# Kernel tuning notes

Measured on AMD Instinct MI355X. Metric: run time of the kernel, lower is better.

## Reference

```python
import jax, jax.numpy as jnp
import numpy as np

NPOINT, NSAMPLE, NKNN = 512, 16, 16


def _fps(xyz, npoint):
    # furthest point sampling. xyz: (B, N, 3) -> idx (B, npoint). Start at index 0 (as in pointnet2 CUDA op).
    B, N, _ = xyz.shape
    def body(carry, _):
        min_d, farthest = carry
        centroid = jnp.take_along_axis(xyz, farthest[:, None, None], axis=1)  # (B,1,3)
        d = jnp.sum((xyz - centroid) ** 2, axis=-1)                            # (B,N)
        min_d = jnp.minimum(min_d, d)
        nxt = jnp.argmax(min_d, axis=-1).astype(jnp.int32)
        return (min_d, nxt), farthest
    init = (jnp.full((B, N), 1e10, xyz.dtype), jnp.zeros((B,), jnp.int32))
    _, idx = jax.lax.scan(body, init, None, length=npoint)
    return jnp.transpose(idx)  # (B, npoint)


def _knn_idx(k, ref, query):
    # k nearest neighbors of each query point among ref points. ref:(B,N,3) query:(B,M,3) -> (B,M,k)
    d = (jnp.sum(query ** 2, -1, keepdims=True)
         - 2.0 * jnp.einsum('bmc,bnc->bmn', query, ref)
         + jnp.sum(ref ** 2, -1)[:, None, :])
    _, idx = jax.lax.top_k(-d, k)
    return idx


def _group(points, idx):
    # grouping_operation: points (B,C,N), idx (B,M,K) -> (B,C,M,K)
    return jax.vmap(lambda p, i: p[:, i])(points, idx)


def _conv1d(x, w, b):  # 1x1 conv: x (B,Cin,N), w (Cout,Cin)
    return jnp.einsum('oc,bcn->bon', w, x) + b[None, :, None]


def _conv2d(x, w, b):  # 1x1 conv: x (B,Cin,M,K)
    return jnp.einsum('oc,bcmk->bomk', w, x) + b[None, :, None, None]


def _linear(x, w, b):
    return x @ w.T + b


def _lrelu(x):
    return jnp.where(x >= 0, x, 0.2 * x)


def _model(point_cloud, sa_w1, sa_b1, sa_w2, sa_b2,
           t_start_w, t_start_b, t_q_w, t_q_b, t_k_w, t_k_b, t_v_w, t_v_b,
           t_pos_w1, t_pos_b1, t_pos_w2, t_pos_b2,
           t_attn_w1, t_attn_b1, t_attn_w2, t_attn_b2, t_end_w, t_end_b,
           exp_w1, exp_b1, exp_w2, exp_b2,
           mlp_w1, mlp_b1, mlp_w2, mlp_b2, mlp_w3, mlp_b3, mlp_w4, mlp_b4):
    B = point_cloud.shape[0]
    xyz = jnp.transpose(point_cloud, (0, 2, 1))                 # (B,N,3)

    # ---- PointNet_SA_Module_KNN (sample_and_group_knn, use_xyz=True) ----
    fps_idx = _fps(xyz, NPOINT)
    new_xyz = jnp.take_along_axis(xyz, fps_idx[:, :, None], axis=1)   # (B,512,3)
    idx = _knn_idx(NSAMPLE, xyz, new_xyz)                             # (B,512,16)
    grouped = _group(point_cloud, idx)                                # (B,3,512,16)
    grouped_xyz_rel = grouped - jnp.transpose(new_xyz, (0, 2, 1))[:, :, :, None]
    new_points = jnp.concatenate([grouped_xyz_rel, grouped], axis=1)  # (B,6,512,16)
    h = jax.nn.relu(_conv2d(new_points, sa_w1, sa_b1))
    h = _conv2d(h, sa_w2, sa_b2)                                      # (B,128,512,16)
    keyfeatures = jnp.max(h, axis=3)                                  # (B,128,512)
    keypoints = jnp.transpose(new_xyz, (0, 2, 1))                     # (B,3,512)

    # ---- point Transformer (BatchNorm in eval with default stats == identity) ----
    identity = keyfeatures
    x = _conv1d(keyfeatures, t_start_w, t_start_b)                    # (B,64,512)
    pos = keypoints
    pos_f = jnp.transpose(pos, (0, 2, 1))                             # (B,512,3)
    idx_knn = _knn_idx(NKNN, pos_f, pos_f)                            # (B,512,16)
    key_g = _group(_conv1d(x, t_k_w, t_k_b), idx_knn)                 # (B,64,512,16)
    value = _conv1d(x, t_v_w, t_v_b)
    query = _conv1d(x, t_q_w, t_q_b)
    qk_rel = query[:, :, :, None] - key_g
    pos_rel = pos[:, :, :, None] - _group(pos, idx_knn)               # (B,3,512,16)
    pe = _conv2d(jax.nn.relu(_conv2d(pos_rel, t_pos_w1, t_pos_b1)), t_pos_w2, t_pos_b2)
    attn = _conv2d(jax.nn.relu(_conv2d(qk_rel + pe, t_attn_w1, t_attn_b1)), t_attn_w2, t_attn_b2)
    attn = jax.nn.softmax(attn, axis=-1)                              # (B,64,512,16)
    v = value[:, :, :, None] + pe
    agg = jnp.sum(attn * v, axis=-1)                                  # (B,64,512)
    keyfeatures = _conv1d(agg, t_end_w, t_end_b) + identity           # (B,128,512)

    # ---- expanding MLP_CONV + global feature fusion ----
    feat = _conv1d(jax.nn.relu(_conv1d(keyfeatures, exp_w1, exp_b1)), exp_w2, exp_b2)  # (B,512,512)
    feat = jnp.transpose(feat, (0, 2, 1))                             # (B,512pts,512ch)
    gf = jnp.max(feat, axis=1, keepdims=True)
    feat = jnp.concatenate([feat, jnp.broadcast_to(gf, feat.shape)], axis=-1)  # (B,512,1024)

    h = _lrelu(_linear(feat, mlp_w1, mlp_b1))
    h = _lrelu(_linear(h, mlp_w2, mlp_b2))
    h = _lrelu(_linear(h, mlp_w3, mlp_b3))
    ret = _linear(h, mlp_w4, mlp_b4)                                  # (B,512,12)
    R = ret[:, :, :9].reshape(B, NPOINT, 3, 3)
    T = ret[:, :, 9:]
    kp = jnp.transpose(keypoints, (0, 2, 1))                          # (B,512,3)
    sym = jnp.einsum('bnc,bncd->bnd', kp, R) + T                      # (B,512,3)
    sym = jnp.transpose(sym, (0, 2, 1))                               # (B,3,512)
    coarse = jnp.concatenate([sym, keypoints], axis=-1)               # (B,3,1024)
    return coarse, sym, keyfeatures


_PARAM_SHAPES = [
    ('sa_w1', (64, 6)), ('sa_b1', (64,)), ('sa_w2', (128, 64)), ('sa_b2', (128,)),
    ('t_start_w', (64, 128)), ('t_start_b', (64,)),
    ('t_q_w', (64, 64)), ('t_q_b', (64,)), ('t_k_w', (64, 64)), ('t_k_b', (64,)),
    ('t_v_w', (64, 64)), ('t_v_b', (64,)),
    ('t_pos_w1', (64, 3)), ('t_pos_b1', (64,)), ('t_pos_w2', (64, 64)), ('t_pos_b2', (64,)),
    ('t_attn_w1', (256, 64)), ('t_attn_b1', (256,)), ('t_attn_w2', (64, 256)), ('t_attn_b2', (64,)),
    ('t_end_w', (128, 64)), ('t_end_b', (128,)),
    ('exp_w1', (256, 128)), ('exp_b1', (256,)), ('exp_w2', (512, 256)), ('exp_b2', (512,)),
    ('mlp_w1', (512, 1024)), ('mlp_b1', (512,)), ('mlp_w2', (256, 512)), ('mlp_b2', (256,)),
    ('mlp_w3', (128, 256)), ('mlp_b3', (128,)), ('mlp_w4', (12, 128)), ('mlp_b4', (12,)),
]


def setup_inputs() -> dict:
    key = jax.random.key(0)
    ks = iter(jax.random.split(key, len(_PARAM_SHAPES) + 1))
    inp = {'point_cloud': jax.random.normal(next(ks), (32, 3, 2048), jnp.float32)}
    for name, shape in _PARAM_SHAPES:
        inp[name] = jax.random.normal(next(ks), shape, jnp.float32) * 0.05
    return inp


def reference(point_cloud, sa_w1, sa_b1, sa_w2, sa_b2,
              t_start_w, t_start_b, t_q_w, t_q_b, t_k_w, t_k_b, t_v_w, t_v_b,
              t_pos_w1, t_pos_b1, t_pos_w2, t_pos_b2,
              t_attn_w1, t_attn_b1, t_attn_w2, t_attn_b2, t_end_w, t_end_b,
              exp_w1, exp_b1, exp_w2, exp_b2,
              mlp_w1, mlp_b1, mlp_w2, mlp_b2, mlp_w3, mlp_b3, mlp_w4, mlp_b4):
    return _model(point_cloud, sa_w1, sa_b1, sa_w2, sa_b2,
                  t_start_w, t_start_b, t_q_w, t_q_b, t_k_w, t_k_b, t_v_w, t_v_b,
                  t_pos_w1, t_pos_b1, t_pos_w2, t_pos_b2,
                  t_attn_w1, t_attn_b1, t_attn_w2, t_attn_b2, t_end_w, t_end_b,
                  exp_w1, exp_b1, exp_w2, exp_b2,
                  mlp_w1, mlp_b1, mlp_w2, mlp_b2, mlp_w3, mlp_b3, mlp_w4, mlp_b4)
```

## Files before the change

kernel.cpp:

```cpp
#include <hip/hip_runtime.h>
#include <math.h>


#define B_ 32
#define N_ 2048
#define NPOINT 512
#define NSAMPLE 16
#define NKNN 16
#define NPTS (B_ * NPOINT)

#define WS_BQKV     0
#define WS_XYZW     872448
#define WS_NEWXYZ   1134592
#define WS_IDX1     1183744
#define WS_IDXK     1445888
#define WS_KF       1708032
#define WS_Q        3805184
#define WS_KFF      7999488
#define WS_E1       10096640
#define WS_FEAT     14290944
#define WS_GF       22679552
#define WS_TOTAL    22695936
#define WS_WFRAG    WS_KFF
#define WS_NXYZW    (WS_KFF + 32768)
#define WS_PD1      WS_FEAT
#define WS_PI1      (WS_FEAT + 2097152)
#define WS_PD2      WS_E1
#define WS_PI2      (WS_E1 + 1048576)

#define UF_E1   40960
#define UF_E2   73728
#define UF_M1   204800
#define UF_M2   729088
#define UF_M3   860160
#define UF_SA1  892928
#define UF_SA2  894976
#define UF_END  903168
#define UF_QKV  911360
#define UB_KFB  3416064
#define UB_QKV  7610368
#define UB_KFF  16261120
#define UB_E1   20193280
#define UB_M2   24387584
#define UB_FEAT 28581888
#define UB_M1   36970496

typedef __attribute__((ext_vector_type(8))) short bf16x8;
typedef __attribute__((ext_vector_type(8))) unsigned short u16x8;
typedef __attribute__((ext_vector_type(4))) float f32x4;

__device__ __forceinline__ unsigned short f2bf(float f) {
  unsigned u = __float_as_uint(f);
  u += 0x7fff + ((u >> 16) & 1);
  return (unsigned short)(u >> 16);
}
__device__ __forceinline__ float bf2f(unsigned short u) {
  return __uint_as_float((unsigned)u << 16);
}
__device__ __forceinline__ unsigned encf(float f) {
  unsigned b = __float_as_uint(f);
  return b ^ (unsigned)(((int)b >> 31) | 0x80000000);
}
__device__ __forceinline__ float decenc(unsigned u) {
  unsigned b = (u & 0x80000000u) ? (u ^ 0x80000000u) : ~u;
  return __uint_as_float(b);
}

#define MFMA16(a, b, c) __builtin_amdgcn_mfma_f32_16x16x32_bf16((a), (b), (c), 0, 0, 0)
#define LDS_FENCE() __asm__ volatile("" ::: "memory")

__device__ __forceinline__ unsigned long long wave_max_u64(unsigned long long key) {
#define DPP_STEP(ctrl) {                                                      \
    int lo = (int)(unsigned)key;                                              \
    int hi = (int)(unsigned)(key >> 32);                                      \
    int plo = __builtin_amdgcn_update_dpp(lo, lo, ctrl, 0xf, 0xf, false);     \
    int phi = __builtin_amdgcn_update_dpp(hi, hi, ctrl, 0xf, 0xf, false);     \
    unsigned long long pk = ((unsigned long long)(unsigned)phi << 32) |       \
                            (unsigned)plo;                                    \
    key = pk > key ? pk : key; }
  DPP_STEP(0x111)
  DPP_STEP(0x112)
  DPP_STEP(0x114)
  DPP_STEP(0x118)
  DPP_STEP(0x142)
  DPP_STEP(0x143)
#undef DPP_STEP
  return key;
}

__device__ __forceinline__ void packw(int u, const float* __restrict__ W, int K,
                                      int N16, unsigned short* __restrict__ dst) {
  int l = u & 63;
  int ntk = u >> 6;
  int nt = ntk & (N16 - 1);
  int kt = ntk / N16;
  int n = nt * 16 + (l & 15);
  int kb = kt * 32 + (l >> 4) * 8;
  const float* s = W + (size_t)n * K + kb;
  unsigned short* d = dst + (size_t)u * 8;
#pragma unroll
  for (int j = 0; j < 8; ++j) d[j] = f2bf(s[j]);
}

__device__ void setup_body(int f,
    const float* __restrict__ pc,
    const float* __restrict__ w_start, const float* __restrict__ w_q,
    const float* __restrict__ w_k, const float* __restrict__ w_v,
    const float* __restrict__ bst, const float* __restrict__ bq,
    const float* __restrict__ bk, const float* __restrict__ bv,
    const float* __restrict__ w1a, const float* __restrict__ w2a,
    const float* __restrict__ wp2,
    const float* __restrict__ we1, const float* __restrict__ we2,
    const float* __restrict__ wm1, const float* __restrict__ wm2,
    const float* __restrict__ wm3,
    const float* __restrict__ sw1, const float* __restrict__ sw2,
    const float* __restrict__ wend,
    float* __restrict__ ws) {
  if (f < 65536) {
    int b = f >> 11, j = f & 2047;
    const float* base = pc + (size_t)b * 3 * 2048;
    float x = base[j], y = base[2048 + j], z = base[4096 + j];
    *(float4*)(ws + WS_XYZW + (size_t)f * 4) = make_float4(x, y, z, x * x + y * y + z * z);
    return;
  }
  int u = f - 65536;
  unsigned short* ws_us = (unsigned short*)ws;
  unsigned short* wf = (unsigned short*)(ws + WS_WFRAG);
  if (u < 2048)  { packw(u, w1a, 64, 16, wf); return; }
  u -= 2048;
  if (u < 2048)  { packw(u, w2a, 256, 4, wf + 16384); return; }
  u -= 2048;
  if (u < 512)   { packw(u, wp2, 64, 4, wf + 32768); return; }
  u -= 512;
  if (u < 4096)  { packw(u, we1, 128, 16, ws_us + UF_E1); return; }
  u -= 4096;
  if (u < 16384) { packw(u, we2, 256, 32, ws_us + UF_E2); return; }
  u -= 16384;
  if (u < 65536) { packw(u, wm1, 1024, 32, ws_us + UF_M1); return; }
  u -= 65536;
  if (u < 16384) { packw(u, wm2, 512, 16, ws_us + UF_M2); return; }
  u -= 16384;
  if (u < 4096)  { packw(u, wm3, 256, 8, ws_us + UF_M3); return; }
  u -= 4096;
  if (u < 256) {
    int l = u & 63, nt = (u >> 6) & 3;
    int n = nt * 16 + (l & 15);
    int kb = (l >> 4) * 8;
    unsigned short* d = ws_us + UF_SA1 + (size_t)u * 8;
#pragma unroll
    for (int j = 0; j < 8; ++j) {
      int k = kb + j;
      d[j] = (k < 6) ? f2bf(sw1[n * 6 + k]) : 0;
    }
    return;
  }
  u -= 256;
  if (u < 1024)  { packw(u, sw2, 64, 8, ws_us + UF_SA2); return; }
  u -= 1024;
  if (u < 1024)  { packw(u, wend, 64, 8, ws_us + UF_END); return; }
  u -= 1024;
  if (u < 4096) {
    int l = u & 63;
    int ntk = u >> 6;
    int nt = ntk & 15;
    int kt = ntk >> 4;
    int n = nt * 16 + (l & 15);
    int kb = kt * 32 + (l >> 4) * 8;
    unsigned short* d = ws_us + UF_QKV + (size_t)u * 8;
    if (n >= 192) {
#pragma unroll
      for (int j = 0; j < 8; ++j) d[j] = 0;
      return;
    }
    const float* wsel = (n < 64) ? w_q : ((n < 128) ? w_k : w_v);
    int nn = n & 63;
#pragma unroll
    for (int j = 0; j < 8; ++j) {
      int k = kb + j;
      float acc = 0.f;
      for (int c = 0; c < 64; ++c)
        acc += wsel[nn * 64 + c] * w_start[c * 128 + k];
      d[j] = f2bf(acc);
    }
    return;
  }
  u -= 4096;
  if (u < 256) {
    float v = 0.f;
    if (u < 192) {
      const float* wsel = (u < 64) ? w_q : ((u < 128) ? w_k : w_v);
      const float* bsel = (u < 64) ? bq : ((u < 128) ? bk : bv);
      int nn = u & 63;
      float acc = bsel[nn];
      for (int c = 0; c < 64; ++c) acc += wsel[nn * 64 + c] * bst[c];
      v = acc;
    }
    ws[WS_BQKV + u] = v;
    return;
  }
  u -= 256;
  if (u < 16384) { ((unsigned*)(ws + WS_GF))[u] = 0; return; }
}

__device__ void fps_body(int b, int t, const float* __restrict__ pc,
                         float* __restrict__ new_xyz,
                         float4* __restrict__ new_xyzw,
                         float4* __restrict__ pts,
                         unsigned long long* __restrict__ kbuf,
                         int* __restrict__ farrec) {
  const float* pb = pc + (size_t)b * 6144;
#pragma unroll
  for (int r = 0; r < 8; ++r) {
    int j = t + r * 256;
    float x = pb[j], y = pb[2048 + j], z = pb[4096 + j];
    pts[j] = make_float4(x, y, z, x * x + y * y + z * z);
  }
  __syncthreads();
  int w = t >> 6, l = t & 63;
  int base = w * 512 + l;
  float px[8], py[8], pz[8], md[8];
#pragma unroll
  for (int r = 0; r < 8; ++r) {
    float4 p = pts[base + r * 64];
    px[r] = p.x; py[r] = p.y; pz[r] = p.z;
    md[r] = 1e10f;
  }
  int far = 0;
  for (int i = 0; i < 512; ++i) {
    float4 cpt = pts[far];
    if (t == 0) farrec[i] = far;
    unsigned long long kk[8];
#pragma unroll
    for (int r = 0; r < 8; ++r) {
      float dx = px[r] - cpt.x, dy = py[r] - cpt.y, dz = pz[r] - cpt.z;
      float d = dx * dx + dy * dy + dz * dz;
      float m = fminf(md[r], d);
      md[r] = m;
      kk[r] = ((unsigned long long)__float_as_uint(m) << 32)
              | (unsigned)(2047 - (base + r * 64));
    }
#pragma unroll
    for (int s = 4; s > 0; s >>= 1)
#pragma unroll
      for (int r = 0; r < s; ++r) kk[r] = kk[r + s] > kk[r] ? kk[r + s] : kk[r];
    unsigned long long key = wave_max_u64(kk[0]);
    if (l == 63) kbuf[(i & 1) * 4 + w] = key;
    __syncthreads();
    const unsigned long long* kb = kbuf + (i & 1) * 4;
    unsigned long long k0 = kb[0], k1 = kb[1], k2 = kb[2], k3 = kb[3];
    k0 = k1 > k0 ? k1 : k0;
    k2 = k3 > k2 ? k3 : k2;
    k0 = k2 > k0 ? k2 : k0;
    far = 2047 - (int)(unsigned)(k0 & 0xffffffffull);
  }
  __syncthreads();
  for (int i = t; i < 512; i += 256) {
    float4 c = pts[farrec[i]];
    new_xyzw[(size_t)b * 512 + i] = c;
    float* o = new_xyz + (size_t)(b * 512 + i) * 3;
    o[0] = c.x; o[1] = c.y; o[2] = c.z;
  }
}

__global__ __launch_bounds__(256) void fps_setup_kernel(
    const float* __restrict__ pc,
    const float* __restrict__ w_start, const float* __restrict__ w_q,
    const float* __restrict__ w_k, const float* __restrict__ w_v,
    const float* __restrict__ bst, const float* __restrict__ bq,
    const float* __restrict__ bk, const float* __restrict__ bv,
    const float* __restrict__ w1a, const float* __restrict__ w2a,
    const float* __restrict__ wp2,
    const float* __restrict__ we1, const float* __restrict__ we2,
    const float* __restrict__ wm1, const float* __restrict__ wm2,
    const float* __restrict__ wm3,
    const float* __restrict__ sw1, const float* __restrict__ sw2,
    const float* __restrict__ wend,
    float* __restrict__ ws,
    float* __restrict__ new_xyz, float4* __restrict__ new_xyzw) {
  __shared__ __align__(16) float4 pts[2048];
  __shared__ unsigned long long kbuf[8];
  __shared__ int farrec[512];
  if (blockIdx.x < 32) {
    fps_body(blockIdx.x, threadIdx.x, pc, new_xyz, new_xyzw, pts, kbuf, farrec);
    return;
  }
  setup_body((blockIdx.x - 32) * 256 + threadIdx.x, pc, w_start, w_q, w_k, w_v,
             bst, bq, bk, bv, w1a, w2a, wp2, we1, we2, wm1, wm2, wm3,
             sw1, sw2, wend, ws);
}

template <int CHSZ, int NCH>
__device__ __forceinline__ void knn_chunk_body(int bid, int tid,
                                               const float4* __restrict__ refs_all,
                                               int refs_per_batch,
                                               const float4* __restrict__ query,
                                               float* __restrict__ pd,
                                               int* __restrict__ pi) {
  int qb = bid & 63, ch = bid >> 6;
  int q = qb * 256 + tid;
  int b = q >> 9;
  const float4* refs = refs_all + (size_t)b * refs_per_batch + ch * CHSZ;
  float4 qp = query[q];
  float qq = qp.w;
  float bd[16]; int bi[16];
#pragma unroll
  for (int s = 0; s < 16; ++s) { bd[s] = 3.0e38f; bi[s] = 0; }
  for (int j = 0; j < CHSZ; ++j) {
    float4 r = refs[j];
    float d = (qq - 2.0f * (qp.x * r.x + qp.y * r.y + qp.z * r.z)) + r.w;
    if (d < bd[15]) {
      float nd = d; int ni = ch * CHSZ + j;
#pragma unroll
      for (int s = 0; s < 16; ++s) {
        bool sw = nd < bd[s];
        float ob = bd[s]; int oi = bi[s];
        bd[s] = sw ? nd : ob; bi[s] = sw ? ni : oi;
        nd = sw ? ob : nd; ni = sw ? oi : ni;
      }
    }
  }
  float* pdq = pd + ((size_t)q * NCH + ch) * 16;
  int* piq = pi + ((size_t)q * NCH + ch) * 16;
#pragma unroll
  for (int s = 0; s < 16; ++s) { pdq[s] = bd[s]; piq[s] = bi[s]; }
}

template <int NCH>
__device__ __forceinline__ void knn_merge_body(int bid, int tid,
                                               const float* __restrict__ pd,
                                               const int* __restrict__ pi,
                                               int* __restrict__ idx) {
  int q = bid * 256 + tid;
  const float* d0 = pd + (size_t)q * NCH * 16;
  const int* i0 = pi + (size_t)q * NCH * 16;
  float bd[16]; int bi[16];
#pragma unroll
  for (int s = 0; s < 16; ++s) { bd[s] = d0[s]; bi[s] = i0[s]; }
  for (int c = 1; c < NCH; ++c) {
    const float* dc = d0 + c * 16;
    const int* ic = i0 + c * 16;
    for (int s = 0; s < 16; ++s) {
      float d = dc[s];
      if (d >= bd[15]) break;
      float nd = d; int ni = ic[s];
#pragma unroll
      for (int k = 0; k < 16; ++k) {
        bool sw = nd < bd[k];
        float ob = bd[k]; int oi = bi[k];
        bd[k] = sw ? nd : ob; bi[k] = sw ? ni : oi;
        nd = sw ? ob : nd; ni = sw ? oi : ni;
      }
    }
  }
#pragma unroll
  for (int s = 0; s < 16; ++s) idx[(size_t)q * 16 + s] = bi[s];
}

__global__ __launch_bounds__(256) void knn1_chunk_kernel(const float4* __restrict__ xyzw,
                                                         const float4* __restrict__ nxyzw,
                                                         float* __restrict__ pd,
                                                         int* __restrict__ pi) {
  knn_chunk_body<256, 8>(blockIdx.x, threadIdx.x, xyzw, 2048, nxyzw, pd, pi);
}

__global__ __launch_bounds__(256) void combo1_kernel(const float4* __restrict__ nxyzw,
                                                     const float* __restrict__ pd1,
                                                     const int* __restrict__ pi1,
                                                     int* __restrict__ idx1,
                                                     float* __restrict__ pd2,
                                                     int* __restrict__ pi2) {
  if (blockIdx.x < 256)
    knn_chunk_body<128, 4>(blockIdx.x, threadIdx.x, nxyzw, 512, nxyzw, pd2, pi2);
  else
    knn_merge_body<8>(blockIdx.x - 256, threadIdx.x, pd1, pi1, idx1);
}

__device__ __forceinline__ void sa_body(int bid, int t,
                                        const float4* __restrict__ xyzw,
                                        const float* __restrict__ new_xyz,
                                        const int* __restrict__ idx1,
                                        const unsigned short* __restrict__ sa1f,
                                        const unsigned short* __restrict__ sa2f,
                                        const float* __restrict__ b1g,
                                        const float* __restrict__ b2g,
                                        unsigned short* __restrict__ kfb,
                                        unsigned short* __restrict__ h1buf) {
  int w = t >> 6, l = t & 63, x = l & 15, quad = l >> 4;
  int pt = bid * 4 + w;
  int b = pt >> 9;
  int jn = idx1[(size_t)pt * 16 + x];
  float4 n4 = xyzw[(size_t)b * 2048 + jn];
  float c0 = new_xyz[(size_t)pt * 3 + 0];
  float c1 = new_xyz[(size_t)pt * 3 + 1];
  float c2 = new_xyz[(size_t)pt * 3 + 2];
  const f32x4 zero = {0.f, 0.f, 0.f, 0.f};
  bf16x8 xf;
#pragma unroll
  for (int j = 0; j < 8; ++j) xf[j] = 0;
  if (quad == 0) {
    xf[0] = (short)f2bf(n4.x - c0);
    xf[1] = (short)f2bf(n4.y - c1);
    xf[2] = (short)f2bf(n4.z - c2);
    xf[3] = (short)f2bf(n4.x);
    xf[4] = (short)f2bf(n4.y);
    xf[5] = (short)f2bf(n4.z);
  }
  unsigned short* hb = h1buf + w * 16 * 72;
#pragma unroll
  for (int nt = 0; nt < 4; ++nt) {
    f32x4 h = MFMA16(xf, *(const bf16x8*)(sa1f + (nt * 64 + l) * 8), zero);
    float bb = b1g[nt * 16 + x];
#pragma unroll
    for (int r = 0; r < 4; ++r)
      hb[(quad * 4 + r) * 72 + nt * 16 + x] = f2bf(fmaxf(h[r] + bb, 0.0f));
  }
  LDS_FENCE();
  bf16x8 hA0 = *(const bf16x8*)(hb + x * 72 + quad * 8);
  bf16x8 hA1 = *(const bf16x8*)(hb + x * 72 + 32 + quad * 8);
  f32x4 acc[8];
#pragma unroll
  for (int nt = 0; nt < 8; ++nt)
    acc[nt] = MFMA16(hA0, *(const bf16x8*)(sa2f + (nt * 64 + l) * 8), zero);
#pragma unroll
  for (int nt = 0; nt < 8; ++nt)
    acc[nt] = MFMA16(hA1, *(const bf16x8*)(sa2f + ((8 + nt) * 64 + l) * 8), acc[nt]);
#pragma unroll
  for (int nt = 0; nt < 8; ++nt) {
    float bb = b2g[nt * 16 + x];
    float m = fmaxf(fmaxf(acc[nt][0], acc[nt][1]), fmaxf(acc[nt][2], acc[nt][3])) + bb;
    m = fmaxf(m, __shfl_xor(m, 16));
    m = fmaxf(m, __shfl_xor(m, 32));
    if (quad == 0) kfb[(size_t)pt * 128 + nt * 16 + x] = f2bf(m);
  }
}

__global__ __launch_bounds__(256) void combo2_kernel(const float4* __restrict__ xyzw,
                                                     const float* __restrict__ new_xyz,
                                                     const int* __restrict__ idx1,
                                                     const unsigned short* __restrict__ sa1f,
                                                     const unsigned short* __restrict__ sa2f,
                                                     const float* __restrict__ b1g,
                                                     const float* __restrict__ b2g,
                                                     unsigned short* __restrict__ kfb,
                                                     const float* __restrict__ pd2,
                                                     const int* __restrict__ pi2,
                                                     int* __restrict__ idxk) {
  __shared__ __align__(16) unsigned short h1buf[4 * 16 * 72];
  if (blockIdx.x < 4096)
    sa_body(blockIdx.x, threadIdx.x, xyzw, new_xyz, idx1, sa1f, sa2f, b1g, b2g,
            kfb, h1buf);
  else
    knn_merge_body<4>(blockIdx.x - 4096, threadIdx.x, pd2, pi2, idxk);
}

__global__ __launch_bounds__(256) void attn_mfma_kernel(
    const unsigned short* __restrict__ qkv, const unsigned short* __restrict__ kfb,
    const int* __restrict__ idx_knn, const float* __restrict__ new_xyz,
    const unsigned short* __restrict__ wfrag,
    const float* __restrict__ ba1, const float* __restrict__ ba2,
    const float* __restrict__ wp1, const float* __restrict__ bp1,
    const float* __restrict__ bp2,
    const unsigned short* __restrict__ wendf, const float* __restrict__ bend,
    unsigned short* __restrict__ kffb, float* __restrict__ out2) {
  const int t = threadIdx.x;
  const int w = t >> 6, l = t & 63;
  const int x = l & 15, quad = l >> 4;
  const unsigned short* w1f = wfrag;
  const unsigned short* w2f = wfrag + 16384;
  const unsigned short* wpf = wfrag + 32768;

  __shared__ float4 wp14[64];
  __shared__ float bp2s[64], ba2s[64], ba1s[256];
  __shared__ __align__(16) float pebuf[4][16 * 68];
  __shared__ __align__(16) unsigned short a1buf[4][16 * 264];
  __shared__ __align__(16) unsigned short aggs[16 * 72];

  if (t < 64) wp14[t] = make_float4(wp1[t * 3], wp1[t * 3 + 1], wp1[t * 3 + 2], bp1[t]);
  else if (t < 128) bp2s[t - 64] = bp2[t - 64];
  else if (t < 192) ba2s[t - 128] = ba2[t - 128];
  if (t < 256) ba1s[t] = ba1[t];
  __syncthreads();

  float* pew = pebuf[w];
  unsigned short* a1w = a1buf[w];
  const f32x4 zero = {0.f, 0.f, 0.f, 0.f};

  for (int pi = 0; pi < 4; ++pi) {
    int pt = blockIdx.x * 16 + w * 4 + pi;
    int b = pt >> 9;
    int jn = idx_knn[(size_t)pt * 16 + x];
    const float* nb = new_xyz + (size_t)(b * 512 + jn) * 3;
    const float* p0 = new_xyz + (size_t)pt * 3;
    float prx = p0[0] - nb[0], pry = p0[1] - nb[1], prz = p0[2] - nb[2];

    bf16x8 hA0, hA1;
#pragma unroll
    for (int j = 0; j < 8; ++j) {
      float4 cf = wp14[quad * 8 + j];
      hA0[j] = (short)f2bf(fmaxf(cf.w + cf.x * prx + cf.y * pry + cf.z * prz, 0.0f));
      float4 cg = wp14[32 + quad * 8 + j];
      hA1[j] = (short)f2bf(fmaxf(cg.w + cg.x * prx + cg.y * pry + cg.z * prz, 0.0f));
    }
    f32x4 pacc[4];
#pragma unroll
    for (int nt = 0; nt < 4; ++nt) {
      bf16x8 b0 = *(const bf16x8*)(wpf + nt * 512 + l * 8);
      bf16x8 b1 = *(const bf16x8*)(wpf + (4 + nt) * 512 + l * 8);
      f32x4 z = MFMA16(hA0, b0, zero);
      pacc[nt] = MFMA16(hA1, b1, z);
    }
    float pev[4][4];
#pragma unroll
    for (int nt = 0; nt < 4; ++nt) {
      float bb = bp2s[nt * 16 + x];
#pragma unroll
      for (int r = 0; r < 4; ++r) {
        float pe = pacc[nt][r] + bb;
        pev[nt][r] = pe;
        pew[(quad * 4 + r) * 68 + nt * 16 + x] = pe;
      }
    }
    LDS_FENCE();

    const unsigned short* qp = qkv + (size_t)pt * 256;
    const unsigned short* kgp = qkv + (size_t)(b * 512 + jn) * 256 + 64;
    const float* per = pew + x * 68;
    u16x8 qa = *(const u16x8*)(qp + quad * 8);
    u16x8 qb = *(const u16x8*)(qp + 32 + quad * 8);
    u16x8 ka = *(const u16x8*)(kgp + quad * 8);
    u16x8 kb = *(const u16x8*)(kgp + 32 + quad * 8);
    float4 p0a = *(const float4*)(per + quad * 8);
    float4 p0b = *(const float4*)(per + quad * 8 + 4);
    float4 p1a = *(const float4*)(per + 32 + quad * 8);
    float4 p1b = *(const float4*)(per + 32 + quad * 8 + 4);
    float pA[8] = {p0a.x, p0a.y, p0a.z, p0a.w, p0b.x, p0b.y, p0b.z, p0b.w};
    float pB[8] = {p1a.x, p1a.y, p1a.z, p1a.w, p1b.x, p1b.y, p1b.z, p1b.w};
    bf16x8 tA0, tA1;
#pragma unroll
    for (int j = 0; j < 8; ++j) {
      tA0[j] = (short)f2bf(bf2f(qa[j]) - bf2f(ka[j]) + pA[j]);
      tA1[j] = (short)f2bf(bf2f(qb[j]) - bf2f(kb[j]) + pB[j]);
    }

    f32x4 acc1[16];
#pragma unroll
    for (int nt = 0; nt < 16; ++nt) {
      bf16x8 bfr = *(const bf16x8*)(w1f + nt * 512 + l * 8);
      acc1[nt] = MFMA16(tA0, bfr, zero);
    }
#pragma unroll
    for (int nt = 0; nt < 16; ++nt) {
      bf16x8 bfr = *(const bf16x8*)(w1f + (16 + nt) * 512 + l * 8);
      acc1[nt] = MFMA16(tA1, bfr, acc1[nt]);
    }
#pragma unroll
    for (int nt = 0; nt < 16; ++nt) {
      float bb = ba1s[nt * 16 + x];
#pragma unroll
      for (int r = 0; r < 4; ++r) {
        a1w[(quad * 4 + r) * 264 + nt * 16 + x] = f2bf(fmaxf(acc1[nt][r] + bb, 0.0f));
      }
    }
    LDS_FENCE();

    f32x4 acc2[4] = {zero, zero, zero, zero};
#pragma unroll
    for (int kt = 0; kt < 8; ++kt) {
      bf16x8 aF = *(const bf16x8*)(a1w + x * 264 + kt * 32 + quad * 8);
#pragma unroll
      for (int nt = 0; nt < 4; ++nt) {
        bf16x8 bfr = *(const bf16x8*)(w2f + (kt * 4 + nt) * 512 + l * 8);
        acc2[nt] = MFMA16(aF, bfr, acc2[nt]);
      }
    }
    LDS_FENCE();

    float aggv[4];
#pragma unroll
    for (int nt = 0; nt < 4; ++nt) {
      float bb = ba2s[nt * 16 + x];
      float vc = bf2f(qkv[(size_t)pt * 256 + 128 + nt * 16 + x]);
      float lg[4];
#pragma unroll
      for (int r = 0; r < 4; ++r) lg[r] = acc2[nt][r] + bb;
      float m = fmaxf(fmaxf(lg[0], lg[1]), fmaxf(lg[2], lg[3]));
      m = fmaxf(m, __shfl_xor(m, 16));
      m = fmaxf(m, __shfl_xor(m, 32));
      float den = 0.f, num = 0.f;
#pragma unroll
      for (int r = 0; r < 4; ++r) {
        float e = __expf(lg[r] - m);
        den += e;
        num += e * (vc + pev[nt][r]);
      }
      den += __shfl_xor(den, 16); den += __shfl_xor(den, 32);
      num += __shfl_xor(num, 16); num += __shfl_xor(num, 32);
      aggv[nt] = num / den;
    }
    float outv = aggv[0];
    if (quad == 1) outv = aggv[1];
    else if (quad == 2) outv = aggv[2];
    else if (quad == 3) outv = aggv[3];
    aggs[(w * 4 + pi) * 72 + l] = f2bf(outv);
  }
  __syncthreads();

  int pt0 = blockIdx.x * 16;
  bf16x8 aF0 = *(const bf16x8*)(aggs + x * 72 + quad * 8);
  bf16x8 aF1 = *(const bf16x8*)(aggs + x * 72 + 32 + quad * 8);
#pragma unroll
  for (int nt2 = 0; nt2 < 2; ++nt2) {
    int nt = w * 2 + nt2;
    f32x4 acc = MFMA16(aF0, *(const bf16x8*)(wendf + (size_t)(0 * 8 + nt) * 512 + l * 8), zero);
    acc = MFMA16(aF1, *(const bf16x8*)(wendf + (size_t)(1 * 8 + nt) * 512 + l * 8), acc);
    int col = nt * 16 + x;
    float bb = bend[col];
#pragma unroll
    for (int r = 0; r < 4; ++r) {
      int pt = pt0 + quad * 4 + r;
      float val = acc[r] + bb + bf2f(kfb[(size_t)pt * 128 + col]);
      kffb[(size_t)pt * 128 + col] = f2bf(val);
      int b = pt >> 9, n = pt & 511;
      out2[(size_t)b * 65536 + (size_t)col * 512 + n] = val;
    }
  }
}

template <int ACT, bool CONCAT, bool GFMAX, bool FINAL>
__global__ __launch_bounds__(256) void gemm_bf16_kernel(
    const unsigned short* __restrict__ A, const unsigned short* __restrict__ Bf,
    const float* __restrict__ bias, unsigned short* __restrict__ C,
    int M, int N, int K, const unsigned* __restrict__ gfenc_in,
    unsigned* __restrict__ gfenc_out,
    const float* __restrict__ w4, const float* __restrict__ b4,
    const float* __restrict__ new_xyz,
    float* __restrict__ out0, float* __restrict__ out1) {
  extern __shared__ __align__(16) char gsm[];
  float* gls = (float*)gsm;
  unsigned short* tile = (unsigned short*)(gsm + 1024);
  float* w4s = (float*)(gsm + 1024 + 128 * 132 * 2);
  float* b4s = w4s + 1536;
  int t = threadIdx.x;
  int l = t & 63, w = t >> 6;
  int x = l & 15, quad = l >> 4;
  int m0 = blockIdx.x * 128 + (w >> 1) * 64;
  int n0 = blockIdx.y * 128 + (w & 1) * 64;
  int N16 = N >> 4;
  if (FINAL) {
    for (int i = t; i < 1536; i += 256) w4s[i] = w4[i];
    if (t < 12) b4s[t] = b4[t];
  }
  const f32x4 zero = {0.f, 0.f, 0.f, 0.f};
  f32x4 acc[4][4];
#pragma unroll
  for (int i = 0; i < 4; ++i)
#pragma unroll
    for (int j = 0; j < 4; ++j) acc[i][j] = zero;

  for (int k0 = 0; k0 < K; k0 += 32) {
    bf16x8 af[4], bfr[4];
#pragma unroll
    for (int mi = 0; mi < 4; ++mi) {
      int arow = m0 + mi * 16 + x;
      if (CONCAT && k0 >= 512) {
        const unsigned* gp = gfenc_in + (size_t)(arow >> 9) * 512 + (k0 - 512) + quad * 8;
        uint4 u0 = *(const uint4*)gp;
        uint4 u1 = *(const uint4*)(gp + 4);
        bf16x8 tv;
        tv[0] = (short)f2bf(decenc(u0.x)); tv[1] = (short)f2bf(decenc(u0.y));
        tv[2] = (short)f2bf(decenc(u0.z)); tv[3] = (short)f2bf(decenc(u0.w));
        tv[4] = (short)f2bf(decenc(u1.x)); tv[5] = (short)f2bf(decenc(u1.y));
        tv[6] = (short)f2bf(decenc(u1.z)); tv[7] = (short)f2bf(decenc(u1.w));
        af[mi] = tv;
      } else {
        const unsigned short* ap;
        if (CONCAT) ap = A + (size_t)arow * 512 + k0 + quad * 8;
        else ap = A + (size_t)arow * K + k0 + quad * 8;
        af[mi] = *(const bf16x8*)ap;
      }
    }
    int bbase = (k0 >> 5) * N16 + (n0 >> 4);
#pragma unroll
    for (int ni = 0; ni < 4; ++ni)
      bfr[ni] = *(const bf16x8*)(Bf + (size_t)(bbase + ni) * 512 + l * 8);
#pragma unroll
    for (int mi = 0; mi < 4; ++mi)
#pragma unroll
      for (int ni = 0; ni < 4; ++ni) acc[mi][ni] = MFMA16(af[mi], bfr[ni], acc[mi][ni]);
  }
  float colmax[4] = {-3.0e38f, -3.0e38f, -3.0e38f, -3.0e38f};
#pragma unroll
  for (int ni = 0; ni < 4; ++ni) {
    int col = n0 + ni * 16 + x;
    float bb = bias[col];
#pragma unroll
    for (int mi = 0; mi < 4; ++mi) {
      int row = m0 + mi * 16 + quad * 4;
#pragma unroll
      for (int r = 0; r < 4; ++r) {
        float v = acc[mi][ni][r] + bb;
        if (ACT == 1) v = fmaxf(v, 0.0f);
        if (ACT == 2) v = (v >= 0.0f) ? v : 0.2f * v;
        if (GFMAX) colmax[ni] = fmaxf(colmax[ni], v);
        if (FINAL) {
          int lrow = (row + r) - blockIdx.x * 128;
          int lcol = col - blockIdx.y * 128;
          tile[lrow * 132 + lcol] = f2bf(v);
        } else {
          C[(size_t)(row + r) * N + col] = f2bf(v);
        }
      }
    }
  }
  if (GFMAX) {
#pragma unroll
    for (int ni = 0; ni < 4; ++ni) {
      float m = colmax[ni];
      m = fmaxf(m, __shfl_xor(m, 16));
      m = fmaxf(m, __shfl_xor(m, 32));
      if (quad == 0) gls[(w >> 1) * 128 + (w & 1) * 64 + ni * 16 + x] = m;
    }
    __syncthreads();
    if (t < 128) {
      float m = fmaxf(gls[t], gls[128 + t]);
      int bidx = (blockIdx.x * 128) >> 9;
      atomicMax(gfenc_out + (size_t)bidx * 512 + blockIdx.y * 128 + t, encf(m));
    }
  }
  if (FINAL) {
    __syncthreads();
    if (t < 128) {
      int gid = blockIdx.x * 128 + t;
      float facc[12];
#pragma unroll
      for (int o = 0; o < 12; ++o) facc[o] = b4s[o];
      const unsigned short* trow = tile + t * 132;
      for (int k = 0; k < 128; k += 4) {
        float x0 = bf2f(trow[k]), x1 = bf2f(trow[k + 1]);
        float x2 = bf2f(trow[k + 2]), x3 = bf2f(trow[k + 3]);
#pragma unroll
        for (int o = 0; o < 12; ++o) {
          facc[o] += x0 * w4s[o * 128 + k] + x1 * w4s[o * 128 + k + 1] +
                     x2 * w4s[o * 128 + k + 2] + x3 * w4s[o * 128 + k + 3];
        }
      }
      float kx = new_xyz[(size_t)gid * 3 + 0];
      float ky = new_xyz[(size_t)gid * 3 + 1];
      float kz = new_xyz[(size_t)gid * 3 + 2];
      int b = gid >> 9, n = gid & 511;
#pragma unroll
      for (int d = 0; d < 3; ++d) {
        float s = kx * facc[d] + ky * facc[3 + d] + kz * facc[6 + d] + facc[9 + d];
        float kp = (d == 0) ? kx : ((d == 1) ? ky : kz);
        out0[(size_t)b * 3072 + (size_t)d * 1024 + n] = s;
        out0[(size_t)b * 3072 + (size_t)d * 1024 + 512 + n] = kp;
        out1[(size_t)b * 1536 + (size_t)d * 512 + n] = s;
      }
    }
  }
}

extern "C" void kernel_launch(void* const* d_in, const int* in_sizes, int n_in,
                              void* d_out, int out_size, void* d_ws, size_t ws_size,
                              hipStream_t stream) {
  (void)in_sizes; (void)n_in; (void)out_size; (void)ws_size;
  const float* pc        = (const float*)d_in[0];
  const float* sa_w1     = (const float*)d_in[1];
  const float* sa_b1     = (const float*)d_in[2];
  const float* sa_w2     = (const float*)d_in[3];
  const float* sa_b2     = (const float*)d_in[4];
  const float* t_start_w = (const float*)d_in[5];
  const float* t_start_b = (const float*)d_in[6];
  const float* t_q_w     = (const float*)d_in[7];
  const float* t_q_b     = (const float*)d_in[8];
  const float* t_k_w     = (const float*)d_in[9];
  const float* t_k_b     = (const float*)d_in[10];
  const float* t_v_w     = (const float*)d_in[11];
  const float* t_v_b     = (const float*)d_in[12];
  const float* t_pos_w1  = (const float*)d_in[13];
  const float* t_pos_b1  = (const float*)d_in[14];
  const float* t_pos_w2  = (const float*)d_in[15];
  const float* t_pos_b2  = (const float*)d_in[16];
  const float* t_attn_w1 = (const float*)d_in[17];
  const float* t_attn_b1 = (const float*)d_in[18];
  const float* t_attn_w2 = (const float*)d_in[19];
  const float* t_attn_b2 = (const float*)d_in[20];
  const float* t_end_w   = (const float*)d_in[21];
  const float* t_end_b   = (const float*)d_in[22];
  const float* exp_w1    = (const float*)d_in[23];
  const float* exp_b1    = (const float*)d_in[24];
  const float* exp_w2    = (const float*)d_in[25];
  const float* exp_b2    = (const float*)d_in[26];
  const float* mlp_w1    = (const float*)d_in[27];
  const float* mlp_b1    = (const float*)d_in[28];
  const float* mlp_w2    = (const float*)d_in[29];
  const float* mlp_b2    = (const float*)d_in[30];
  const float* mlp_w3    = (const float*)d_in[31];
  const float* mlp_b3    = (const float*)d_in[32];
  const float* mlp_w4    = (const float*)d_in[33];
  const float* mlp_b4    = (const float*)d_in[34];

  float* ws = (float*)d_ws;
  unsigned short* ws_us = (unsigned short*)d_ws;
  unsigned* gfenc = (unsigned*)(ws + WS_GF);
  float* out = (float*)d_out;
  float* out0 = out;
  float* out1 = out + 98304;
  float* out2 = out + 147456;

  fps_setup_kernel<<<812, 256, 0, stream>>>(pc, t_start_w, t_q_w, t_k_w, t_v_w,
                                            t_start_b, t_q_b, t_k_b, t_v_b,
                                            t_attn_w1, t_attn_w2, t_pos_w2,
                                            exp_w1, exp_w2, mlp_w1, mlp_w2, mlp_w3,
                                            sa_w1, sa_w2, t_end_w, ws,
                                            ws + WS_NEWXYZ, (float4*)(ws + WS_NXYZW));
  knn1_chunk_kernel<<<512, 256, 0, stream>>>((const float4*)(ws + WS_XYZW),
                                             (const float4*)(ws + WS_NXYZW),
                                             ws + WS_PD1, (int*)(ws + WS_PI1));
  combo1_kernel<<<320, 256, 0, stream>>>((const float4*)(ws + WS_NXYZW),
                                         ws + WS_PD1, (const int*)(ws + WS_PI1),
                                         (int*)(ws + WS_IDX1),
                                         ws + WS_PD2, (int*)(ws + WS_PI2));
  combo2_kernel<<<4160, 256, 0, stream>>>((const float4*)(ws + WS_XYZW), ws + WS_NEWXYZ,
                                          (const int*)(ws + WS_IDX1),
                                          ws_us + UF_SA1, ws_us + UF_SA2,
                                          sa_b1, sa_b2, ws_us + UB_KFB,
                                          ws + WS_PD2, (const int*)(ws + WS_PI2),
                                          (int*)(ws + WS_IDXK));
  gemm_bf16_kernel<0, false, false, false><<<dim3(128, 2), 256, 1024, stream>>>(
      ws_us + UB_KFB, ws_us + UF_QKV, ws + WS_BQKV, ws_us + UB_QKV,
      NPTS, 256, 128, nullptr, nullptr, nullptr, nullptr, nullptr, nullptr, nullptr);
  attn_mfma_kernel<<<1024, 256, 0, stream>>>(ws_us + UB_QKV, ws_us + UB_KFB,
                                             (const int*)(ws + WS_IDXK), ws + WS_NEWXYZ,
                                             (const unsigned short*)(ws + WS_WFRAG),
                                             t_attn_b1, t_attn_b2,
                                             t_pos_w1, t_pos_b1, t_pos_b2,
                                             ws_us + UF_END, t_end_b,
                                             ws_us + UB_KFF, out2);
  gemm_bf16_kernel<1, false, false, false><<<dim3(128, 2), 256, 1024, stream>>>(
      ws_us + UB_KFF, ws_us + UF_E1, exp_b1, ws_us + UB_E1, NPTS, 256, 128,
      nullptr, nullptr, nullptr, nullptr, nullptr, nullptr, nullptr);
  gemm_bf16_kernel<0, false, true, false><<<dim3(128, 4), 256, 1024, stream>>>(
      ws_us + UB_E1, ws_us + UF_E2, exp_b2, ws_us + UB_FEAT, NPTS, 512, 256,
      nullptr, gfenc, nullptr, nullptr, nullptr, nullptr, nullptr);
  gemm_bf16_kernel<2, true, false, false><<<dim3(128, 4), 256, 1024, stream>>>(
      ws_us + UB_FEAT, ws_us + UF_M1, mlp_b1, ws_us + UB_M1, NPTS, 512, 1024,
      gfenc, nullptr, nullptr, nullptr, nullptr, nullptr, nullptr);
  gemm_bf16_kernel<2, false, false, false><<<dim3(128, 2), 256, 1024, stream>>>(
      ws_us + UB_M1, ws_us + UF_M2, mlp_b2, ws_us + UB_M2, NPTS, 256, 512,
      nullptr, nullptr, nullptr, nullptr, nullptr, nullptr, nullptr);
  gemm_bf16_kernel<2, false, false, true><<<dim3(128, 1), 256, 41008, stream>>>(
      ws_us + UB_M2, ws_us + UF_M3, mlp_b3, nullptr, NPTS, 128, 256,
      nullptr, nullptr, mlp_w4, mlp_b4, ws + WS_NEWXYZ, out0, out1);
}
```

Measured before the change: 794.0 us.

## Regroup KNN chunk and merge stages into separate combined launches

The kernel groupings change. Both KNN chunk stages (the 2048-point and the 512-point searches) now run in one launch, both merge stages run in a second launch, and the SA MLP gets a dedicated third launch. Before, the second chunk stage shared a launch with the first merge, and the second merge shared a launch with the SA MLP. The aim is to balance work across blocks and keep the light merge blocks from mixing with the heavy SA blocks, at the cost of a different dependency schedule between stages.

```diff
diff --git a/kernel.cpp b/kernel.cpp
--- a/kernel.cpp
+++ b/kernel.cpp
@@ -356,37 +356,42 @@
   for (int s = 0; s < 16; ++s) idx[(size_t)q * 16 + s] = bi[s];
 }
 
-__global__ __launch_bounds__(256) void knn1_chunk_kernel(const float4* __restrict__ xyzw,
+__global__ __launch_bounds__(256) void knn_chunks_kernel(const float4* __restrict__ xyzw,
                                                          const float4* __restrict__ nxyzw,
-                                                         float* __restrict__ pd,
-                                                         int* __restrict__ pi) {
-  knn_chunk_body<256, 8>(blockIdx.x, threadIdx.x, xyzw, 2048, nxyzw, pd, pi);
-}
-
-__global__ __launch_bounds__(256) void combo1_kernel(const float4* __restrict__ nxyzw,
-                                                     const float* __restrict__ pd1,
-                                                     const int* __restrict__ pi1,
-                                                     int* __restrict__ idx1,
-                                                     float* __restrict__ pd2,
-                                                     int* __restrict__ pi2) {
-  if (blockIdx.x < 256)
-    knn_chunk_body<128, 4>(blockIdx.x, threadIdx.x, nxyzw, 512, nxyzw, pd2, pi2);
+                                                         float* __restrict__ pd1,
+                                                         int* __restrict__ pi1,
+                                                         float* __restrict__ pd2,
+                                                         int* __restrict__ pi2) {
+  if (blockIdx.x < 512)
+    knn_chunk_body<256, 8>(blockIdx.x, threadIdx.x, xyzw, 2048, nxyzw, pd1, pi1);
   else
-    knn_merge_body<8>(blockIdx.x - 256, threadIdx.x, pd1, pi1, idx1);
-}
-
-__device__ __forceinline__ void sa_body(int bid, int t,
-                                        const float4* __restrict__ xyzw,
-                                        const float* __restrict__ new_xyz,
-                                        const int* __restrict__ idx1,
-                                        const unsigned short* __restrict__ sa1f,
-                                        const unsigned short* __restrict__ sa2f,
-                                        const float* __restrict__ b1g,
-                                        const float* __restrict__ b2g,
-                                        unsigned short* __restrict__ kfb,
-                                        unsigned short* __restrict__ h1buf) {
+    knn_chunk_body<128, 4>(blockIdx.x - 512, threadIdx.x, nxyzw, 512, nxyzw, pd2, pi2);
+}
+
+__global__ __launch_bounds__(256) void knn_merges_kernel(const float* __restrict__ pd1,
+                                                         const int* __restrict__ pi1,
+                                                         int* __restrict__ idx1,
+                                                         const float* __restrict__ pd2,
+                                                         const int* __restrict__ pi2,
+                                                         int* __restrict__ idxk) {
+  if (blockIdx.x < 64)
+    knn_merge_body<8>(blockIdx.x, threadIdx.x, pd1, pi1, idx1);
+  else
+    knn_merge_body<4>(blockIdx.x - 64, threadIdx.x, pd2, pi2, idxk);
+}
+
+__global__ __launch_bounds__(256) void sa_kernel(const float4* __restrict__ xyzw,
+                                                 const float* __restrict__ new_xyz,
+                                                 const int* __restrict__ idx1,
+                                                 const unsigned short* __restrict__ sa1f,
+                                                 const unsigned short* __restrict__ sa2f,
+                                                 const float* __restrict__ b1g,
+                                                 const float* __restrict__ b2g,
+                                                 unsigned short* __restrict__ kfb) {
+  __shared__ __align__(16) unsigned short h1buf[4 * 16 * 72];
+  int t = threadIdx.x;
   int w = t >> 6, l = t & 63, x = l & 15, quad = l >> 4;
-  int pt = bid * 4 + w;
+  int pt = blockIdx.x * 4 + w;
   int b = pt >> 9;
   int jn = idx1[(size_t)pt * 16 + x];
   float4 n4 = xyzw[(size_t)b * 2048 + jn];
@@ -432,25 +437,6 @@
     m = fmaxf(m, __shfl_xor(m, 32));
     if (quad == 0) kfb[(size_t)pt * 128 + nt * 16 + x] = f2bf(m);
   }
-}
-
-__global__ __launch_bounds__(256) void combo2_kernel(const float4* __restrict__ xyzw,
-                                                     const float* __restrict__ new_xyz,
-                                                     const int* __restrict__ idx1,
-                                                     const unsigned short* __restrict__ sa1f,
-                                                     const unsigned short* __restrict__ sa2f,
-                                                     const float* __restrict__ b1g,
-                                                     const float* __restrict__ b2g,
-                                                     unsigned short* __restrict__ kfb,
-                                                     const float* __restrict__ pd2,
-                                                     const int* __restrict__ pi2,
-                                                     int* __restrict__ idxk) {
-  __shared__ __align__(16) unsigned short h1buf[4 * 16 * 72];
-  if (blockIdx.x < 4096)
-    sa_body(blockIdx.x, threadIdx.x, xyzw, new_xyz, idx1, sa1f, sa2f, b1g, b2g,
-            kfb, h1buf);
-  else
-    knn_merge_body<4>(blockIdx.x - 4096, threadIdx.x, pd2, pi2, idxk);
 }
 
 __global__ __launch_bounds__(256) void attn_mfma_kernel(
@@ -814,19 +800,18 @@
                                             exp_w1, exp_w2, mlp_w1, mlp_w2, mlp_w3,
                                             sa_w1, sa_w2, t_end_w, ws,
                                             ws + WS_NEWXYZ, (float4*)(ws + WS_NXYZW));
-  knn1_chunk_kernel<<<512, 256, 0, stream>>>((const float4*)(ws + WS_XYZW),
+  knn_chunks_kernel<<<768, 256, 0, stream>>>((const float4*)(ws + WS_XYZW),
                                              (const float4*)(ws + WS_NXYZW),
-                                             ws + WS_PD1, (int*)(ws + WS_PI1));
-  combo1_kernel<<<320, 256, 0, stream>>>((const float4*)(ws + WS_NXYZW),
-                                         ws + WS_PD1, (const int*)(ws + WS_PI1),
-                                         (int*)(ws + WS_IDX1),
-                                         ws + WS_PD2, (int*)(ws + WS_PI2));
-  combo2_kernel<<<4160, 256, 0, stream>>>((const float4*)(ws + WS_XYZW), ws + WS_NEWXYZ,
-                                          (const int*)(ws + WS_IDX1),
-                                          ws_us + UF_SA1, ws_us + UF_SA2,
-                                          sa_b1, sa_b2, ws_us + UB_KFB,
-                                          ws + WS_PD2, (const int*)(ws + WS_PI2),
-                                          (int*)(ws + WS_IDXK));
+                                             ws + WS_PD1, (int*)(ws + WS_PI1),
+                                             ws + WS_PD2, (int*)(ws + WS_PI2));
+  knn_merges_kernel<<<128, 256, 0, stream>>>(ws + WS_PD1, (const int*)(ws + WS_PI1),
+                                             (int*)(ws + WS_IDX1),
+                                             ws + WS_PD2, (const int*)(ws + WS_PI2),
+                                             (int*)(ws + WS_IDXK));
+  sa_kernel<<<4096, 256, 0, stream>>>((const float4*)(ws + WS_XYZW), ws + WS_NEWXYZ,
+                                      (const int*)(ws + WS_IDX1),
+                                      ws_us + UF_SA1, ws_us + UF_SA2,
+                                      sa_b1, sa_b2, ws_us + UB_KFB);
   gemm_bf16_kernel<0, false, false, false><<<dim3(128, 2), 256, 1024, stream>>>(
       ws_us + UB_KFB, ws_us + UF_QKV, ws + WS_BQKV, ws_us + UB_QKV,
       NPTS, 256, 128, nullptr, nullptr, nullptr, nullptr, nullptr, nullptr, nullptr);
```

Result: faster. 754.2 us (-5.0%).
